# Optimization experiments

Hardware: AMD Instinct MI355X
Metric: run time of the kernel (lower is better)

## Reference

```python
import jax, jax.numpy as jnp
import numpy as np
import math

EMBED = 1024
HEADS = 16
HEAD_DIM = EMBED // HEADS
B, S = 2, 2048


def setup_inputs() -> dict:
    key = jax.random.key(0)
    ks = jax.random.split(key, 11)
    s = 1.0 / math.sqrt(EMBED)
    return {
        "query": jax.random.normal(ks[0], (B, S, EMBED), jnp.float32),
        "key_": jax.random.normal(ks[1], (B, S, EMBED), jnp.float32),
        "value": jax.random.normal(ks[2], (B, S, EMBED), jnp.float32),
        "Wq": jax.random.normal(ks[3], (EMBED, EMBED), jnp.float32) * s,
        "bq": jax.random.normal(ks[4], (EMBED,), jnp.float32) * s,
        "Wk": jax.random.normal(ks[5], (EMBED, EMBED), jnp.float32) * s,
        "bk": jax.random.normal(ks[6], (EMBED,), jnp.float32) * s,
        "Wv": jax.random.normal(ks[7], (EMBED, EMBED), jnp.float32) * s,
        "bv": jax.random.normal(ks[8], (EMBED,), jnp.float32) * s,
        "Wo": jax.random.normal(ks[9], (EMBED, EMBED), jnp.float32) * s,
        "bo": jax.random.normal(ks[10], (EMBED,), jnp.float32) * s,
    }


def reference(query, key_, value, Wq, bq, Wk, bk, Wv, bv, Wo, bo):
    b, s, e = query.shape
    # projections (torch Linear: x @ W.T + b)
    q = query @ Wq.T + bq
    k = key_ @ Wk.T + bk
    v = value @ Wv.T + bv
    # [B, H, S, hd]
    q = q.reshape(b, s, HEADS, HEAD_DIM).transpose(0, 2, 1, 3)
    k = k.reshape(b, s, HEADS, HEAD_DIM).transpose(0, 2, 1, 3)
    v = v.reshape(b, s, HEADS, HEAD_DIM).transpose(0, 2, 1, 3)
    scores = jnp.einsum("bhqd,bhkd->bhqk", q, k) / math.sqrt(HEAD_DIM)
    attn = jax.nn.softmax(scores, axis=-1)
    out = jnp.einsum("bhqk,bhkd->bhqd", attn, v)
    out = out.transpose(0, 2, 1, 3).reshape(b, s, e)
    return out @ Wo.T + bo
```

## Files before the change

### kernel.cpp

```cpp
#include <hip/hip_runtime.h>
#include <hip/hip_bf16.h>

using bf16_t = __bf16;
using bf16x4 = __attribute__((ext_vector_type(4))) __bf16;
using bf16x8 = __attribute__((ext_vector_type(8))) __bf16;
using f32x4  = __attribute__((ext_vector_type(4))) float;
using u32 = unsigned int;

constexpr int S_ = 2048, E_ = 1024, M_ = 4096;
constexpr size_t MAT_A = (size_t)M_ * E_;
constexpr size_t MAT_W = (size_t)E_ * E_;

__device__ __forceinline__ bf16_t tobf(float f) {
  unsigned u = __builtin_bit_cast(unsigned, f);
  unsigned short r = (unsigned short)((u + 0x7fffu + ((u >> 16) & 1u)) >> 16);
  return __builtin_bit_cast(bf16_t, r);
}
__device__ __forceinline__ u32 packbf2(float a, float b) {
  u32 ua = __builtin_bit_cast(u32, a) + 0x8000u;
  u32 ub = __builtin_bit_cast(u32, b) + 0x8000u;
  return (ua >> 16) | (ub & 0xffff0000u);
}

__device__ __forceinline__ void async_lds16(const bf16_t* g, bf16_t* l) {
  __builtin_amdgcn_global_load_lds(
      (const __attribute__((address_space(1))) unsigned int*)g,
      (__attribute__((address_space(3))) unsigned int*)l, 16, 0, 0);
}

__global__ __launch_bounds__(256) void cvt4k(
    const float* __restrict__ s0, const float* __restrict__ s1,
    const float* __restrict__ s2, const float* __restrict__ s3,
    bf16_t* __restrict__ d0, bf16_t* __restrict__ d1,
    bf16_t* __restrict__ d2, bf16_t* __restrict__ d3) {
  const int w = blockIdx.y;
  const float* s = w == 0 ? s0 : w == 1 ? s1 : w == 2 ? s2 : s3;
  bf16_t* d = w == 0 ? d0 : w == 1 ? d1 : w == 2 ? d2 : d3;
  size_t i = ((size_t)blockIdx.x * 256 + threadIdx.x) * 8;
  float4 a = *(const float4*)(s + i);
  float4 b = *(const float4*)(s + i + 4);
  bf16x8 o;
  o[0] = tobf(a.x); o[1] = tobf(a.y); o[2] = tobf(a.z); o[3] = tobf(a.w);
  o[4] = tobf(b.x); o[5] = tobf(b.y); o[6] = tobf(b.z); o[7] = tobf(b.w);
  *(bf16x8*)(d + i) = o;
}

template <bool OUT_BF16>
__device__ __forceinline__ void gemm_body(const bf16_t* __restrict__ X,
                                          const bf16_t* __restrict__ W,
                                          const float* __restrict__ bias,
                                          void* __restrict__ Cout,
                                          int row0, int col0) {
  constexpr int K = 1024, N = 1024, BK = 32;
  __shared__ __align__(16) bf16_t As[128 * BK];
  __shared__ __align__(16) bf16_t Bs[128 * BK];
  const int tid = threadIdx.x;
  const int lane = tid & 63, wave = tid >> 6;
  const int l15 = lane & 15, q = lane >> 4;
  const int wm = (wave & 1) * 64, wn = (wave >> 1) * 64;
  const f32x4 fzero = {0.f, 0.f, 0.f, 0.f};

  f32x4 acc[4][4];
#pragma unroll
  for (int i = 0; i < 4; ++i)
#pragma unroll
    for (int j = 0; j < 4; ++j) acc[i][j] = fzero;

  const bf16_t* gA = X + (size_t)(row0 + wave * 32 + (lane >> 2)) * K + (lane & 3) * 8;
  const bf16_t* gB = W + (size_t)(col0 + wave * 32 + (lane >> 2)) * K + (lane & 3) * 8;
  bf16_t* lA = As + wave * 32 * BK;
  bf16_t* lB = Bs + wave * 32 * BK;

  for (int k0 = 0; k0 < K; k0 += BK) {
    __syncthreads();
    async_lds16(gA + k0, lA);
    async_lds16(gA + k0 + 16 * K, lA + 16 * BK);
    async_lds16(gB + k0, lB);
    async_lds16(gB + k0 + 16 * K, lB + 16 * BK);
    __syncthreads();
    bf16x8 af[4], bw[4];
#pragma unroll
    for (int i = 0; i < 4; ++i)
      af[i] = *(const bf16x8*)(As + (wm + i * 16 + l15) * BK + q * 8);
#pragma unroll
    for (int j = 0; j < 4; ++j)
      bw[j] = *(const bf16x8*)(Bs + (wn + j * 16 + l15) * BK + q * 8);
#pragma unroll
    for (int i = 0; i < 4; ++i)
#pragma unroll
      for (int j = 0; j < 4; ++j)
        acc[i][j] = __builtin_amdgcn_mfma_f32_16x16x32_bf16(af[i], bw[j],
                                                            acc[i][j], 0, 0, 0);
  }

#pragma unroll
  for (int j = 0; j < 4; ++j) {
    const int col = col0 + wn + j * 16 + l15;
    const float bc = bias[col];
#pragma unroll
    for (int i = 0; i < 4; ++i)
#pragma unroll
      for (int r = 0; r < 4; ++r) {
        const int row = row0 + wm + i * 16 + q * 4 + r;
        const float v = acc[i][j][r] + bc;
        if (OUT_BF16)
          ((bf16_t*)Cout)[(size_t)row * N + col] = tobf(v);
        else
          ((float*)Cout)[(size_t)row * N + col] = v;
      }
  }
}

__global__ __launch_bounds__(256) void gemm_qkv(
    const bf16_t* __restrict__ xq, const bf16_t* __restrict__ xk,
    const bf16_t* __restrict__ xv, const bf16_t* __restrict__ wq,
    const bf16_t* __restrict__ wk, const bf16_t* __restrict__ wv,
    const float* __restrict__ bq, const float* __restrict__ bk,
    const float* __restrict__ bv, bf16_t* __restrict__ outb) {
  const int which = blockIdx.y >> 3;
  const bf16_t* X = which == 0 ? xq : which == 1 ? xk : xv;
  const bf16_t* W = which == 0 ? wq : which == 1 ? wk : wv;
  const float* b = which == 0 ? bq : which == 1 ? bk : bv;
  gemm_body<true>(X, W, b, outb + (size_t)which * MAT_A,
                  blockIdx.x * 128, (blockIdx.y & 7) * 128);
}

__global__ __launch_bounds__(256) void gemm_o(const bf16_t* __restrict__ X,
                                              const bf16_t* __restrict__ W,
                                              const float* __restrict__ b,
                                              float* __restrict__ C) {
  gemm_body<false>(X, W, b, C, blockIdx.x * 128, blockIdx.y * 128);
}

__global__ __launch_bounds__(256) void transpose_v(const bf16_t* __restrict__ V,
                                                   bf16_t* __restrict__ Vt) {
  __shared__ __align__(16) bf16_t Ts[64][72];
  const int tid = threadIdx.x;
  const int bh = blockIdx.y, b = bh >> 4, h = bh & 15;
  const int kt = blockIdx.x * 64;
  const int t = tid >> 3, c8 = (tid & 7) * 8;
  const bf16_t* src = V + ((size_t)(b * S_ + kt + t)) * E_ + h * 64 + c8;
  *(bf16x8*)&Ts[t][c8] = *(const bf16x8*)src;
  *(bf16x8*)&Ts[t + 32][c8] = *(const bf16x8*)(src + (size_t)32 * E_);
  __syncthreads();
  bf16_t* dst = Vt + ((size_t)bh * 64 + t) * S_ + kt + c8;
  bf16x8 o0, o1;
#pragma unroll
  for (int j = 0; j < 8; ++j) o0[j] = Ts[c8 + j][t];
#pragma unroll
  for (int j = 0; j < 8; ++j) o1[j] = Ts[c8 + j][t + 32];
  *(bf16x8*)dst = o0;
  *(bf16x8*)(dst + (size_t)32 * S_) = o1;
}

__global__ __launch_bounds__(256) void attn_mfma(
    const bf16_t* __restrict__ Qm, const bf16_t* __restrict__ Km,
    const bf16_t* __restrict__ Vtg, bf16_t* __restrict__ Om) {
  constexpr int LDP = 72;
  __shared__ __align__(16) bf16_t Ks[64 * 64];
  __shared__ __align__(16) bf16_t Vs[64 * 64];
  __shared__ __align__(16) bf16_t Ps[4][2][16 * LDP];

  const int tid = threadIdx.x, lane = tid & 63, wave = tid >> 6;
  const int l15 = lane & 15, q = lane >> 4;
  const int bh = blockIdx.x & 31, qb = blockIdx.x >> 5;
  const int b = bh >> 4, h = bh & 15;
  const size_t rowbase = (size_t)b * S_;
  const int hcol = h * 64;
  const int q0 = qb * 128 + wave * 32;
  constexpr float SC = 0.18033688011f;

  const int srow = lane >> 3;
  const int schunk = (lane & 7) ^ srow;
  const bf16_t* gK = Km + (rowbase + wave * 8 + srow) * E_ + hcol + schunk * 8;
  const bf16_t* gV = Vtg + ((size_t)bh * 64 + wave * 8 + srow) * S_ + schunk * 8;
  bf16_t* lK = Ks + wave * 512;
  bf16_t* lV = Vs + wave * 512;

  bf16x8 qf[2][2];
#pragma unroll
  for (int qt = 0; qt < 2; ++qt) {
    const bf16_t* qp = Qm + (rowbase + q0 + qt * 16 + l15) * E_ + hcol + q * 8;
    qf[qt][0] = *(const bf16x8*)qp;
    qf[qt][1] = *(const bf16x8*)(qp + 32);
  }

  const f32x4 fzero = {0.f, 0.f, 0.f, 0.f};
  f32x4 oacc[2][4];
#pragma unroll
  for (int qt = 0; qt < 2; ++qt)
#pragma unroll
    for (int mt = 0; mt < 4; ++mt) oacc[qt][mt] = fzero;
  float lsum[2] = {0.f, 0.f};

  const int rbase = l15 * 64;
  int ck[2];
  ck[0] = ((q) ^ (l15 & 7)) * 8;
  ck[1] = ((4 + q) ^ (l15 & 7)) * 8;
  bf16_t* pw0 = Ps[wave][0] + l15 * LDP;
  bf16_t* pw1 = Ps[wave][1] + l15 * LDP;

  for (int kt = 0; kt < S_; kt += 64) {
    __syncthreads();
    async_lds16(gK + (size_t)kt * E_, lK);
    async_lds16(gK + (size_t)(kt + 32) * E_, lK + 32 * 64);
    async_lds16(gV + kt, lV);
    async_lds16(gV + kt + 32 * S_, lV + 32 * 64);
    __syncthreads();

#pragma unroll
    for (int nt = 0; nt < 4; ++nt) {
      bf16x8 a0 = *(const bf16x8*)(Ks + nt * 1024 + rbase + ck[0]);
      bf16x8 a1 = *(const bf16x8*)(Ks + nt * 1024 + rbase + ck[1]);
#pragma unroll
      for (int qt = 0; qt < 2; ++qt) {
        f32x4 st = fzero;
        st = __builtin_amdgcn_mfma_f32_16x16x32_bf16(a0, qf[qt][0], st, 0, 0, 0);
        st = __builtin_amdgcn_mfma_f32_16x16x32_bf16(a1, qf[qt][1], st, 0, 0, 0);
        float p0 = __builtin_amdgcn_exp2f(st[0] * SC);
        float p1 = __builtin_amdgcn_exp2f(st[1] * SC);
        float p2 = __builtin_amdgcn_exp2f(st[2] * SC);
        float p3 = __builtin_amdgcn_exp2f(st[3] * SC);
        lsum[qt] += (p0 + p1) + (p2 + p3);
        uint2 pk;
        pk.x = packbf2(p0, p1);
        pk.y = packbf2(p2, p3);
        *(uint2*)((qt ? pw1 : pw0) + nt * 16 + q * 4) = pk;
      }
    }

#pragma unroll
    for (int kk = 0; kk < 2; ++kk) {
      bf16x8 bp0 = *(const bf16x8*)(pw0 + kk * 32 + q * 8);
      bf16x8 bp1 = *(const bf16x8*)(pw1 + kk * 32 + q * 8);
#pragma unroll
      for (int mt = 0; mt < 4; ++mt) {
        bf16x8 av = *(const bf16x8*)(Vs + mt * 1024 + rbase + ck[kk]);
        oacc[0][mt] = __builtin_amdgcn_mfma_f32_16x16x32_bf16(av, bp0,
                                                              oacc[0][mt], 0, 0, 0);
        oacc[1][mt] = __builtin_amdgcn_mfma_f32_16x16x32_bf16(av, bp1,
                                                              oacc[1][mt], 0, 0, 0);
      }
    }
  }

#pragma unroll
  for (int qt = 0; qt < 2; ++qt) {
    float l = lsum[qt];
    l += __shfl_xor(l, 16);
    l += __shfl_xor(l, 32);
    const float inv = 1.0f / l;
    const size_t orow = (rowbase + q0 + qt * 16 + l15) * E_ + hcol + q * 4;
#pragma unroll
    for (int mt = 0; mt < 4; ++mt) {
      bf16x4 o;
#pragma unroll
      for (int r = 0; r < 4; ++r) o[r] = tobf(oacc[qt][mt][r] * inv);
      *(bf16x4*)(Om + orow + mt * 16) = o;
    }
  }
}

extern "C" void kernel_launch(void* const* d_in, const int* in_sizes, int n_in,
                              void* d_out, int out_size, void* d_ws, size_t ws_size,
                              hipStream_t stream) {
  const float* query = (const float*)d_in[0];
  const float* key_  = (const float*)d_in[1];
  const float* value = (const float*)d_in[2];
  const float* Wq = (const float*)d_in[3];
  const float* bq = (const float*)d_in[4];
  const float* Wk = (const float*)d_in[5];
  const float* bk = (const float*)d_in[6];
  const float* Wv = (const float*)d_in[7];
  const float* bv = (const float*)d_in[8];
  const float* Wo = (const float*)d_in[9];
  const float* bo = (const float*)d_in[10];

  bf16_t* qc  = (bf16_t*)d_ws;
  bf16_t* kc  = qc + MAT_A;
  bf16_t* vc  = kc + MAT_A;
  bf16_t* wqb = vc + MAT_A;
  bf16_t* wkb = wqb + MAT_W;
  bf16_t* wvb = wkb + MAT_W;
  bf16_t* wob = wvb + MAT_W;
  bf16_t* Qb  = wob + MAT_W;
  bf16_t* Kb  = Qb + MAT_A;
  bf16_t* Vb  = Kb + MAT_A;
  bf16_t* Vt  = kc;
  bf16_t* AOb = qc;

  cvt4k<<<dim3(MAT_A / 2048, 3), 256, 0, stream>>>(query, key_, value, value,
                                                   qc, kc, vc, vc);
  cvt4k<<<dim3(MAT_W / 2048, 4), 256, 0, stream>>>(Wq, Wk, Wv, Wo,
                                                   wqb, wkb, wvb, wob);
  gemm_qkv<<<dim3(32, 24), 256, 0, stream>>>(qc, kc, vc, wqb, wkb, wvb,
                                             bq, bk, bv, Qb);
  transpose_v<<<dim3(S_ / 64, 32), 256, 0, stream>>>(Vb, Vt);
  attn_mfma<<<512, 256, 0, stream>>>(Qb, Kb, Vt, AOb);
  gemm_o<<<dim3(32, 8), 256, 0, stream>>>(AOb, wob, bo, (float*)d_out);
}
```

Baseline: 242.8 us.

## Fuse V transpose into QKV GEMM, split attention keys across waves, shrink out-proj tiles

The QKV GEMM epilogue now writes V straight into the head-transposed layout, which removes the separate transpose kernel and its round trip through memory. Attention uses 64-query blocks in which two wave pairs each process half of the key sequence, and the partial outputs and row sums are combined through shared memory at the end. This doubles the grid to 1024 blocks. The output projection uses 64-row tiles, doubling its grid to 512 blocks. Together these aim to raise occupancy and cut launch and memory traffic, at the cost of a shared-memory reduction and strided 8-byte V stores.

Measured after the change: 250.2 us. 3.0% more time.

```diff
diff --git a/kernel.cpp b/kernel.cpp
--- a/kernel.cpp
+++ b/kernel.cpp
@@ -21,7 +21,6 @@
   u32 ub = __builtin_bit_cast(u32, b) + 0x8000u;
   return (ua >> 16) | (ub & 0xffff0000u);
 }
-
 __device__ __forceinline__ void async_lds16(const bf16_t* g, bf16_t* l) {
   __builtin_amdgcn_global_load_lds(
       (const __attribute__((address_space(1))) unsigned int*)g,
@@ -45,137 +44,176 @@
   *(bf16x8*)(d + i) = o;
 }
 
-template <bool OUT_BF16>
-__device__ __forceinline__ void gemm_body(const bf16_t* __restrict__ X,
-                                          const bf16_t* __restrict__ W,
-                                          const float* __restrict__ bias,
-                                          void* __restrict__ Cout,
-                                          int row0, int col0) {
-  constexpr int K = 1024, N = 1024, BK = 32;
-  __shared__ __align__(16) bf16_t As[128 * BK];
-  __shared__ __align__(16) bf16_t Bs[128 * BK];
-  const int tid = threadIdx.x;
-  const int lane = tid & 63, wave = tid >> 6;
-  const int l15 = lane & 15, q = lane >> 4;
-  const int wm = (wave & 1) * 64, wn = (wave >> 1) * 64;
-  const f32x4 fzero = {0.f, 0.f, 0.f, 0.f};
-
-  f32x4 acc[4][4];
-#pragma unroll
-  for (int i = 0; i < 4; ++i)
-#pragma unroll
-    for (int j = 0; j < 4; ++j) acc[i][j] = fzero;
-
-  const bf16_t* gA = X + (size_t)(row0 + wave * 32 + (lane >> 2)) * K + (lane & 3) * 8;
-  const bf16_t* gB = W + (size_t)(col0 + wave * 32 + (lane >> 2)) * K + (lane & 3) * 8;
-  bf16_t* lA = As + wave * 32 * BK;
-  bf16_t* lB = Bs + wave * 32 * BK;
-
-  for (int k0 = 0; k0 < K; k0 += BK) {
-    __syncthreads();
-    async_lds16(gA + k0, lA);
-    async_lds16(gA + k0 + 16 * K, lA + 16 * BK);
-    async_lds16(gB + k0, lB);
-    async_lds16(gB + k0 + 16 * K, lB + 16 * BK);
-    __syncthreads();
-    bf16x8 af[4], bw[4];
-#pragma unroll
-    for (int i = 0; i < 4; ++i)
-      af[i] = *(const bf16x8*)(As + (wm + i * 16 + l15) * BK + q * 8);
-#pragma unroll
-    for (int j = 0; j < 4; ++j)
-      bw[j] = *(const bf16x8*)(Bs + (wn + j * 16 + l15) * BK + q * 8);
-#pragma unroll
-    for (int i = 0; i < 4; ++i)
-#pragma unroll
-      for (int j = 0; j < 4; ++j)
-        acc[i][j] = __builtin_amdgcn_mfma_f32_16x16x32_bf16(af[i], bw[j],
-                                                            acc[i][j], 0, 0, 0);
-  }
-
-#pragma unroll
-  for (int j = 0; j < 4; ++j) {
-    const int col = col0 + wn + j * 16 + l15;
-    const float bc = bias[col];
-#pragma unroll
-    for (int i = 0; i < 4; ++i)
-#pragma unroll
-      for (int r = 0; r < 4; ++r) {
-        const int row = row0 + wm + i * 16 + q * 4 + r;
-        const float v = acc[i][j][r] + bc;
-        if (OUT_BF16)
-          ((bf16_t*)Cout)[(size_t)row * N + col] = tobf(v);
-        else
-          ((float*)Cout)[(size_t)row * N + col] = v;
-      }
-  }
-}
-
 __global__ __launch_bounds__(256) void gemm_qkv(
     const bf16_t* __restrict__ xq, const bf16_t* __restrict__ xk,
     const bf16_t* __restrict__ xv, const bf16_t* __restrict__ wq,
     const bf16_t* __restrict__ wk, const bf16_t* __restrict__ wv,
     const float* __restrict__ bq, const float* __restrict__ bk,
-    const float* __restrict__ bv, bf16_t* __restrict__ outb) {
+    const float* __restrict__ bv, bf16_t* __restrict__ outb,
+    bf16_t* __restrict__ Vt) {
+  constexpr int K = 1024, N = 1024, BK = 32;
+  __shared__ __align__(16) bf16_t As[128 * BK];
+  __shared__ __align__(16) bf16_t Bs[128 * BK];
   const int which = blockIdx.y >> 3;
   const bf16_t* X = which == 0 ? xq : which == 1 ? xk : xv;
   const bf16_t* W = which == 0 ? wq : which == 1 ? wk : wv;
-  const float* b = which == 0 ? bq : which == 1 ? bk : bv;
-  gemm_body<true>(X, W, b, outb + (size_t)which * MAT_A,
-                  blockIdx.x * 128, (blockIdx.y & 7) * 128);
+  const float* bias = which == 0 ? bq : which == 1 ? bk : bv;
+  const int row0 = blockIdx.x * 128, col0 = (blockIdx.y & 7) * 128;
+
+  const int tid = threadIdx.x, lane = tid & 63, wave = tid >> 6;
+  const int l15 = lane & 15, q = lane >> 4;
+  const int wm = (wave & 1) * 64, wn = (wave >> 1) * 64;
+  const f32x4 fzero = {0.f, 0.f, 0.f, 0.f};
+
+  f32x4 acc[4][4];
+#pragma unroll
+  for (int i = 0; i < 4; ++i)
+#pragma unroll
+    for (int j = 0; j < 4; ++j) acc[i][j] = fzero;
+
+  const bf16_t* gA = X + (size_t)(row0 + wave * 32 + (lane >> 2)) * K + (lane & 3) * 8;
+  const bf16_t* gB = W + (size_t)(col0 + wave * 32 + (lane >> 2)) * K + (lane & 3) * 8;
+  bf16_t* lA = As + wave * 32 * BK;
+  bf16_t* lB = Bs + wave * 32 * BK;
+
+  for (int k0 = 0; k0 < K; k0 += BK) {
+    __syncthreads();
+    async_lds16(gA + k0, lA);
+    async_lds16(gA + k0 + 16 * K, lA + 16 * BK);
+    async_lds16(gB + k0, lB);
+    async_lds16(gB + k0 + 16 * K, lB + 16 * BK);
+    __syncthreads();
+    bf16x8 af[4], bw[4];
+#pragma unroll
+    for (int i = 0; i < 4; ++i)
+      af[i] = *(const bf16x8*)(As + (wm + i * 16 + l15) * BK + q * 8);
+#pragma unroll
+    for (int j = 0; j < 4; ++j)
+      bw[j] = *(const bf16x8*)(Bs + (wn + j * 16 + l15) * BK + q * 8);
+#pragma unroll
+    for (int i = 0; i < 4; ++i)
+#pragma unroll
+      for (int j = 0; j < 4; ++j)
+        acc[i][j] = __builtin_amdgcn_mfma_f32_16x16x32_bf16(af[i], bw[j],
+                                                            acc[i][j], 0, 0, 0);
+  }
+
+  if (which < 2) {
+    bf16_t* C = outb + (size_t)which * MAT_A;
+#pragma unroll
+    for (int j = 0; j < 4; ++j) {
+      const int col = col0 + wn + j * 16 + l15;
+      const float bc = bias[col];
+#pragma unroll
+      for (int i = 0; i < 4; ++i)
+#pragma unroll
+        for (int r = 0; r < 4; ++r) {
+          const int row = row0 + wm + i * 16 + q * 4 + r;
+          C[(size_t)row * N + col] = tobf(acc[i][j][r] + bc);
+        }
+    }
+  } else {
+#pragma unroll
+    for (int j = 0; j < 4; ++j) {
+      const int col = col0 + wn + j * 16 + l15;
+      const float bc = bias[col];
+      const int head = col >> 6, d = col & 63;
+#pragma unroll
+      for (int i = 0; i < 4; ++i) {
+        const int row = row0 + wm + i * 16 + q * 4;
+        const int bb = row >> 11, tok = row & 2047;
+        bf16x4 o;
+#pragma unroll
+        for (int r = 0; r < 4; ++r) o[r] = tobf(acc[i][j][r] + bc);
+        *(bf16x4*)(Vt + ((size_t)(bb * 16 + head) * 64 + d) * S_ + tok) = o;
+      }
+    }
+  }
 }
 
 __global__ __launch_bounds__(256) void gemm_o(const bf16_t* __restrict__ X,
                                               const bf16_t* __restrict__ W,
-                                              const float* __restrict__ b,
+                                              const float* __restrict__ bias,
                                               float* __restrict__ C) {
-  gemm_body<false>(X, W, b, C, blockIdx.x * 128, blockIdx.y * 128);
-}
-
-__global__ __launch_bounds__(256) void transpose_v(const bf16_t* __restrict__ V,
-                                                   bf16_t* __restrict__ Vt) {
-  __shared__ __align__(16) bf16_t Ts[64][72];
-  const int tid = threadIdx.x;
-  const int bh = blockIdx.y, b = bh >> 4, h = bh & 15;
-  const int kt = blockIdx.x * 64;
-  const int t = tid >> 3, c8 = (tid & 7) * 8;
-  const bf16_t* src = V + ((size_t)(b * S_ + kt + t)) * E_ + h * 64 + c8;
-  *(bf16x8*)&Ts[t][c8] = *(const bf16x8*)src;
-  *(bf16x8*)&Ts[t + 32][c8] = *(const bf16x8*)(src + (size_t)32 * E_);
-  __syncthreads();
-  bf16_t* dst = Vt + ((size_t)bh * 64 + t) * S_ + kt + c8;
-  bf16x8 o0, o1;
-#pragma unroll
-  for (int j = 0; j < 8; ++j) o0[j] = Ts[c8 + j][t];
-#pragma unroll
-  for (int j = 0; j < 8; ++j) o1[j] = Ts[c8 + j][t + 32];
-  *(bf16x8*)dst = o0;
-  *(bf16x8*)(dst + (size_t)32 * S_) = o1;
+  constexpr int K = 1024, N = 1024, BK = 32;
+  __shared__ __align__(16) bf16_t As[64 * BK];
+  __shared__ __align__(16) bf16_t Bs[128 * BK];
+  const int tid = threadIdx.x, lane = tid & 63, wave = tid >> 6;
+  const int l15 = lane & 15, q = lane >> 4;
+  const int row0 = blockIdx.x * 64, col0 = blockIdx.y * 128;
+  const int wm = (wave & 1) * 32, wn = (wave >> 1) * 64;
+  const f32x4 fzero = {0.f, 0.f, 0.f, 0.f};
+
+  f32x4 acc[2][4];
+#pragma unroll
+  for (int i = 0; i < 2; ++i)
+#pragma unroll
+    for (int j = 0; j < 4; ++j) acc[i][j] = fzero;
+
+  const bf16_t* gA = X + (size_t)(row0 + wave * 16 + (lane >> 2)) * K + (lane & 3) * 8;
+  const bf16_t* gB = W + (size_t)(col0 + wave * 32 + (lane >> 2)) * K + (lane & 3) * 8;
+  bf16_t* lA = As + wave * 16 * BK;
+  bf16_t* lB = Bs + wave * 32 * BK;
+
+  for (int k0 = 0; k0 < K; k0 += BK) {
+    __syncthreads();
+    async_lds16(gA + k0, lA);
+    async_lds16(gB + k0, lB);
+    async_lds16(gB + k0 + 16 * K, lB + 16 * BK);
+    __syncthreads();
+    bf16x8 af[2], bw[4];
+#pragma unroll
+    for (int i = 0; i < 2; ++i)
+      af[i] = *(const bf16x8*)(As + (wm + i * 16 + l15) * BK + q * 8);
+#pragma unroll
+    for (int j = 0; j < 4; ++j)
+      bw[j] = *(const bf16x8*)(Bs + (wn + j * 16 + l15) * BK + q * 8);
+#pragma unroll
+    for (int i = 0; i < 2; ++i)
+#pragma unroll
+      for (int j = 0; j < 4; ++j)
+        acc[i][j] = __builtin_amdgcn_mfma_f32_16x16x32_bf16(af[i], bw[j],
+                                                            acc[i][j], 0, 0, 0);
+  }
+
+#pragma unroll
+  for (int j = 0; j < 4; ++j) {
+    const int col = col0 + wn + j * 16 + l15;
+    const float bc = bias[col];
+#pragma unroll
+    for (int i = 0; i < 2; ++i)
+#pragma unroll
+      for (int r = 0; r < 4; ++r) {
+        const int row = row0 + wm + i * 16 + q * 4 + r;
+        C[(size_t)row * N + col] = acc[i][j][r] + bc;
+      }
+  }
 }
 
 __global__ __launch_bounds__(256) void attn_mfma(
     const bf16_t* __restrict__ Qm, const bf16_t* __restrict__ Km,
     const bf16_t* __restrict__ Vtg, bf16_t* __restrict__ Om) {
   constexpr int LDP = 72;
-  __shared__ __align__(16) bf16_t Ks[64 * 64];
-  __shared__ __align__(16) bf16_t Vs[64 * 64];
+  __shared__ __align__(16) bf16_t Ks[2][64 * 64];
+  __shared__ __align__(16) bf16_t Vs[2][64 * 64];
   __shared__ __align__(16) bf16_t Ps[4][2][16 * LDP];
 
   const int tid = threadIdx.x, lane = tid & 63, wave = tid >> 6;
   const int l15 = lane & 15, q = lane >> 4;
+  const int wr = wave & 1, kh = wave >> 1;
   const int bh = blockIdx.x & 31, qb = blockIdx.x >> 5;
   const int b = bh >> 4, h = bh & 15;
   const size_t rowbase = (size_t)b * S_;
   const int hcol = h * 64;
-  const int q0 = qb * 128 + wave * 32;
+  const int q0 = qb * 64 + wr * 32;
   constexpr float SC = 0.18033688011f;
 
   const int srow = lane >> 3;
   const int schunk = (lane & 7) ^ srow;
-  const bf16_t* gK = Km + (rowbase + wave * 8 + srow) * E_ + hcol + schunk * 8;
-  const bf16_t* gV = Vtg + ((size_t)bh * 64 + wave * 8 + srow) * S_ + schunk * 8;
-  bf16_t* lK = Ks + wave * 512;
-  bf16_t* lV = Vs + wave * 512;
+  const bf16_t* gK = Km + (rowbase + kh * 1024 + wr * 32 + srow) * E_ + hcol + schunk * 8;
+  const bf16_t* gV = Vtg + ((size_t)bh * 64 + wr * 32 + srow) * S_ + kh * 1024 + schunk * 8;
+  bf16_t* lK = Ks[kh] + wr * 32 * 64;
+  bf16_t* lV = Vs[kh] + wr * 32 * 64;
 
   bf16x8 qf[2][2];
 #pragma unroll
@@ -199,19 +237,22 @@
   ck[1] = ((4 + q) ^ (l15 & 7)) * 8;
   bf16_t* pw0 = Ps[wave][0] + l15 * LDP;
   bf16_t* pw1 = Ps[wave][1] + l15 * LDP;
-
-  for (int kt = 0; kt < S_; kt += 64) {
-    __syncthreads();
-    async_lds16(gK + (size_t)kt * E_, lK);
-    async_lds16(gK + (size_t)(kt + 32) * E_, lK + 32 * 64);
-    async_lds16(gV + kt, lV);
-    async_lds16(gV + kt + 32 * S_, lV + 32 * 64);
+  const bf16_t* Kbuf = Ks[kh];
+  const bf16_t* Vbuf = Vs[kh];
+
+  for (int t = 0; t < 16; ++t) {
+    __syncthreads();
+#pragma unroll
+    for (int j = 0; j < 4; ++j) {
+      async_lds16(gK + (size_t)(t * 64 + j * 8) * E_, lK + j * 512);
+      async_lds16(gV + t * 64 + (size_t)(j * 8) * S_, lV + j * 512);
+    }
     __syncthreads();
 
 #pragma unroll
     for (int nt = 0; nt < 4; ++nt) {
-      bf16x8 a0 = *(const bf16x8*)(Ks + nt * 1024 + rbase + ck[0]);
-      bf16x8 a1 = *(const bf16x8*)(Ks + nt * 1024 + rbase + ck[1]);
+      bf16x8 a0 = *(const bf16x8*)(Kbuf + nt * 1024 + rbase + ck[0]);
+      bf16x8 a1 = *(const bf16x8*)(Kbuf + nt * 1024 + rbase + ck[1]);
 #pragma unroll
       for (int qt = 0; qt < 2; ++qt) {
         f32x4 st = fzero;
@@ -235,7 +276,7 @@
       bf16x8 bp1 = *(const bf16x8*)(pw1 + kk * 32 + q * 8);
 #pragma unroll
       for (int mt = 0; mt < 4; ++mt) {
-        bf16x8 av = *(const bf16x8*)(Vs + mt * 1024 + rbase + ck[kk]);
+        bf16x8 av = *(const bf16x8*)(Vbuf + mt * 1024 + rbase + ck[kk]);
         oacc[0][mt] = __builtin_amdgcn_mfma_f32_16x16x32_bf16(av, bp0,
                                                               oacc[0][mt], 0, 0, 0);
         oacc[1][mt] = __builtin_amdgcn_mfma_f32_16x16x32_bf16(av, bp1,
@@ -244,19 +285,39 @@
     }
   }
 
-#pragma unroll
-  for (int qt = 0; qt < 2; ++qt) {
-    float l = lsum[qt];
-    l += __shfl_xor(l, 16);
-    l += __shfl_xor(l, 32);
-    const float inv = 1.0f / l;
-    const size_t orow = (rowbase + q0 + qt * 16 + l15) * E_ + hcol + q * 4;
-#pragma unroll
-    for (int mt = 0; mt < 4; ++mt) {
-      bf16x4 o;
-#pragma unroll
-      for (int r = 0; r < 4; ++r) o[r] = tobf(oacc[qt][mt][r] * inv);
-      *(bf16x4*)(Om + orow + mt * 16) = o;
+  __syncthreads();
+  if (kh == 1) {
+    float* dst = (float*)(wr == 0 ? Ks[0] : Vs[0]);
+#pragma unroll
+    for (int qt = 0; qt < 2; ++qt)
+#pragma unroll
+      for (int mt = 0; mt < 4; ++mt)
+        *(f32x4*)(dst + ((qt * 4 + mt) * 64 + lane) * 4) = oacc[qt][mt];
+    float* lf = (float*)Ps[wave];
+    lf[lane] = lsum[0];
+    lf[64 + lane] = lsum[1];
+  }
+  __syncthreads();
+  if (kh == 0) {
+    const float* src = (const float*)(wr == 0 ? Ks[0] : Vs[0]);
+    const float* lf = (const float*)Ps[wave + 2];
+#pragma unroll
+    for (int qt = 0; qt < 2; ++qt) {
+      float l = lsum[qt] + lf[qt * 64 + lane];
+#pragma unroll
+      for (int mt = 0; mt < 4; ++mt)
+        oacc[qt][mt] += *(const f32x4*)(src + ((qt * 4 + mt) * 64 + lane) * 4);
+      l += __shfl_xor(l, 16);
+      l += __shfl_xor(l, 32);
+      const float inv = 1.0f / l;
+      const size_t orow = (rowbase + q0 + qt * 16 + l15) * E_ + hcol + q * 4;
+#pragma unroll
+      for (int mt = 0; mt < 4; ++mt) {
+        bf16x4 o;
+#pragma unroll
+        for (int r = 0; r < 4; ++r) o[r] = tobf(oacc[qt][mt][r] * inv);
+        *(bf16x4*)(Om + orow + mt * 16) = o;
+      }
     }
   }
 }
@@ -285,17 +346,15 @@
   bf16_t* wob = wvb + MAT_W;
   bf16_t* Qb  = wob + MAT_W;
   bf16_t* Kb  = Qb + MAT_A;
-  bf16_t* Vb  = Kb + MAT_A;
-  bf16_t* Vt  = kc;
-  bf16_t* AOb = qc;
+  bf16_t* Vt  = Kb + MAT_A;
+  bf16_t* AOb = Vt + MAT_A;
 
   cvt4k<<<dim3(MAT_A / 2048, 3), 256, 0, stream>>>(query, key_, value, value,
                                                    qc, kc, vc, vc);
   cvt4k<<<dim3(MAT_W / 2048, 4), 256, 0, stream>>>(Wq, Wk, Wv, Wo,
                                                    wqb, wkb, wvb, wob);
   gemm_qkv<<<dim3(32, 24), 256, 0, stream>>>(qc, kc, vc, wqb, wkb, wvb,
-                                             bq, bk, bv, Qb);
-  transpose_v<<<dim3(S_ / 64, 32), 256, 0, stream>>>(Vb, Vt);
-  attn_mfma<<<512, 256, 0, stream>>>(Qb, Kb, Vt, AOb);
-  gemm_o<<<dim3(32, 8), 256, 0, stream>>>(AOb, wob, bo, (float*)d_out);
-}
+                                             bq, bk, bv, Qb, Vt);
+  attn_mfma<<<1024, 256, 0, stream>>>(Qb, Kb, Vt, AOb);
+  gemm_o<<<dim3(64, 8), 256, 0, stream>>>(AOb, wob, bo, (float*)d_out);
+}
```
